# Kernel tuning notes

Hardware: AMD Instinct MI355X
Metric: run time of the kernel (lower is better)

Reference implementation:

```python
import jax, jax.numpy as jnp
import numpy as np

D = 64; H = 8; HD = 8; L = 3; FFN = 256
MAX_CHUNKS = 1024; MCL = 16


def rms_norm(x, w, eps=1e-6):
    return x * w * jax.lax.rsqrt(jnp.mean(x * x, axis=-1, keepdims=True) + eps)


def rope(x):
    # x: [B, S, H, HD]
    S, hd = x.shape[1], x.shape[-1]
    half = hd // 2
    freqs = 1.0 / (10000.0 ** (jnp.arange(half, dtype=x.dtype) * 2.0 / hd))
    ang = jnp.arange(S, dtype=x.dtype)[:, None] * freqs  # [S, half]
    cos = jnp.cos(ang)[None, :, None, :]
    sin = jnp.sin(ang)[None, :, None, :]
    x1, x2 = x[..., :half], x[..., half:]
    return jnp.concatenate([x1 * cos - x2 * sin, x1 * sin + x2 * cos], axis=-1)


def block(x, wq, wk, wv, wo, g1, g2, w1, w2):
    B, S, _ = x.shape
    h = rms_norm(x, g1)
    q = rope((h @ wq).reshape(B, S, H, HD))
    k = rope((h @ wk).reshape(B, S, H, HD))
    v = (h @ wv).reshape(B, S, H, HD)
    scores = jnp.einsum('bqhd,bkhd->bhqk', q, k) / jnp.sqrt(jnp.asarray(HD, x.dtype))
    causal = jnp.tril(jnp.ones((S, S), dtype=bool))
    scores = jnp.where(causal, scores, jnp.asarray(-1e30, x.dtype))
    attn = jax.nn.softmax(scores, axis=-1)
    o = jnp.einsum('bhqk,bkhd->bqhd', attn, v).reshape(B, S, D)
    x = x + o @ wo
    h2 = rms_norm(x, g2)
    return x + jax.nn.gelu(h2 @ w1, approximate=False) @ w2


def setup_inputs() -> dict:
    key = jax.random.key(0)
    ks = jax.random.split(key, 12)
    B, S = 4, 2048
    s = 1.0 / np.sqrt(D)
    return {
        'x': jax.random.normal(ks[0], (B, S, D), jnp.float32),
        'pad_token_vector': jax.random.normal(ks[1], (D,), jnp.float32),
        'x_ids': jax.random.randint(ks[2], (B, S), 0, 256),
        'pad_token_id': 257,
        'Wq': jax.random.normal(ks[3], (L, D, D), jnp.float32) * s,
        'Wk': jax.random.normal(ks[4], (L, D, D), jnp.float32) * s,
        'Wv': jax.random.normal(ks[5], (L, D, D), jnp.float32) * s,
        'Wo': jax.random.normal(ks[6], (L, D, D), jnp.float32) * s,
        'ln1': jnp.ones((L, D), jnp.float32),
        'ln2': jnp.ones((L, D), jnp.float32),
        'W1': jax.random.normal(ks[7], (L, D, FFN), jnp.float32) * s,
        'W2': jax.random.normal(ks[8], (L, FFN, D), jnp.float32) * (1.0 / np.sqrt(FFN)),
        'Whead': jax.random.normal(ks[9], (D, 2), jnp.float32) * s,
        'bhead': jnp.zeros((2,), jnp.float32),
    }


def reference(x, pad_token_vector, x_ids, pad_token_id, Wq, Wk, Wv, Wo, ln1, ln2, W1, W2, Whead, bhead):
    B, S, _ = x.shape
    h = x
    for l in range(L):
        h = block(h, Wq[l], Wk[l], Wv[l], Wo[l], ln1[l], ln2[l], W1[l], W2[l])
    logits = h @ Whead + bhead  # [B, S, 2]
    end_mask = logits[..., 0] > logits[..., 1]  # [B, S]
    t = jnp.arange(S)
    # fallback: if a row has no end, mark the last position as an end
    has_end = jnp.any(end_mask, axis=-1, keepdims=True)
    end_mask = jnp.where(has_end, end_mask, t[None, :] == S - 1)
    em = end_mask.astype(jnp.int32)
    num_ends = jnp.sum(em, axis=-1)                 # [B] = number of chunks
    chunk_id = jnp.cumsum(em, axis=-1) - em         # exclusive count of prior ends
    prev_end = jnp.concatenate([jnp.ones((B, 1), bool), end_mask[:, :-1]], axis=1)
    start_marker = jnp.where(prev_end, t[None, :], -1)
    start = jax.lax.associative_scan(jnp.maximum, start_marker, axis=-1)  # cummax -> chunk start per token
    pos = t[None, :] - start                        # position within chunk
    valid = (chunk_id < num_ends[:, None]) & (chunk_id < MAX_CHUNKS) & (pos < MCL)
    c_idx = jnp.where(valid, chunk_id, MAX_CHUNKS)  # invalid -> dummy chunk, sliced off
    p_idx = jnp.where(valid, pos, 0)
    b_idx = jnp.arange(B)[:, None]
    out = jnp.broadcast_to(pad_token_vector, (B, MAX_CHUNKS + 1, MCL, D))
    out = out.at[b_idx, c_idx, p_idx].set(h)[:, :MAX_CHUNKS]
    ids = jnp.full((B, MAX_CHUNKS + 1, MCL), pad_token_id, dtype=x_ids.dtype)
    ids = ids.at[b_idx, c_idx, p_idx].set(x_ids)[:, :MAX_CHUNKS]
    reg_term = jnp.mean(logits[..., 1])
    return out, ids, reg_term
```

## Files before the change

### kernel.cpp

```cpp
#include <hip/hip_runtime.h>
#include <math.h>

constexpr int D   = 64;
constexpr int H   = 8;
constexpr int HD  = 8;
constexpr int NL  = 3;
constexpr int FFNx= 256;
constexpr int Bb  = 4;
constexpr int Ss  = 2048;
constexpr int NT  = Bb * Ss;
constexpr int MAXC= 1024;
constexpr int MCL = 16;

constexpr int TPB  = 72;
constexpr int BPB  = 36;
constexpr int PBSZ = 2304;

constexpr size_t WX  = 0;
constexpr size_t WQ  = 524288;
constexpr size_t WKV = 2621440;
constexpr size_t WPB = 4194304;
constexpr size_t WL1 = 9764864;
constexpr size_t WEM = WL1 + NT;
constexpr size_t WINV= WEM + NT;
constexpr size_t WCT = WINV + Bb*MAXC*MCL;
constexpr size_t WST = WCT + Ss*4;

constexpr float LOG2E = 1.4426950408889634f;

typedef float v2f  __attribute__((ext_vector_type(2)));
typedef float f16v __attribute__((ext_vector_type(16)));
using ckv_t = const __attribute__((address_space(4))) f16v*;

__device__ __forceinline__ float rdlane(float v, int l) {
    return __builtin_bit_cast(float, __builtin_amdgcn_readlane(__builtin_bit_cast(int, v), l));
}

__global__ void k_init(const float* __restrict__ x, float* __restrict__ X,
                       float* __restrict__ ct, float* __restrict__ st) {
    int i = blockIdx.x * blockDim.x + threadIdx.x;
    constexpr int N4 = NT * D / 4;
    if (i < N4) ((float4*)X)[i] = ((const float4*)x)[i];
    if (i < Ss * 4) {
        int s = i >> 2, f = i & 3;
        const float fr[4] = {1.0f, 0.1f, 0.01f, 0.001f};
        float ang = (float)s * fr[f];
        ct[i] = cosf(ang);
        st[i] = sinf(ang);
    }
}

__global__ __launch_bounds__(256) void k_qkv(
    const float* __restrict__ X, const float* __restrict__ Wq,
    const float* __restrict__ Wk, const float* __restrict__ Wv,
    const float* __restrict__ g1, const float* __restrict__ ct,
    const float* __restrict__ st, float* __restrict__ Q,
    float* __restrict__ KV) {
    __shared__ float wq_s[D*D], wk_s[D*D], wv_s[D*D];
    __shared__ float g_s[D];
    int tid = threadIdx.x;
    for (int i = tid; i < D*D; i += 256) {
        wq_s[i] = Wq[i]; wk_s[i] = Wk[i]; wv_s[i] = Wv[i];
    }
    if (tid < D) g_s[tid] = g1[tid];
    __syncthreads();
    int w = tid >> 6, d = tid & 63;
    int t0 = blockIdx.x * 16;
    for (int it = 0; it < 4; ++it) {
        int t = t0 + it*4 + w;
        float xv = X[t*D + d];
        float ss = xv * xv;
        #pragma unroll
        for (int off = 32; off; off >>= 1) ss += __shfl_xor(ss, off);
        float r = 1.0f / sqrtf(ss * (1.0f/D) + 1e-6f);
        float h = xv * g_s[d] * r;
        float aq = 0.f, ak = 0.f, av = 0.f;
        #pragma unroll
        for (int j = 0; j < D; ++j) {
            float hj = rdlane(h, j);
            aq += hj * wq_s[j*D + d];
            ak += hj * wk_s[j*D + d];
            av += hj * wv_s[j*D + d];
        }
        int s  = t & (Ss - 1);
        int e  = d & 7;
        int fi = e & 3;
        float c  = ct[s*4 + fi];
        float sn = st[s*4 + fi];
        float pq = __shfl_xor(aq, 4);
        float pk = __shfl_xor(ak, 4);
        float rq, rk;
        if (e < 4) { rq = aq*c - pq*sn; rk = ak*c - pk*sn; }
        else       { rq = pq*sn + aq*c; rk = pk*sn + ak*c; }
        Q[t*D + d] = rq;
        int bq = t >> 11;
        int hh = d >> 3;
        float* kvp = KV + ((((size_t)(bq*H + hh))*Ss + s) << 4);
        kvp[e]     = rk;
        kvp[8 + e] = av;
    }
}

template<int DIAG>
__device__ __forceinline__ void attn_loop4(
    ckv_t kvs, int L, int rel0,
    const v2f* __restrict__ qp0, const v2f* __restrict__ qp1,
    v2f& l0, v2f& l1, v2f* __restrict__ o0, v2f* __restrict__ o1) {
    #pragma unroll 4
    for (int j = 0; j < 64; ++j) {
        f16v kv = kvs[j];
        v2f a1;
        a1  = qp1[0] * (v2f){kv[0], kv[0]};
        a1 += qp1[1] * (v2f){kv[1], kv[1]};
        a1 += qp1[2] * (v2f){kv[2], kv[2]};
        a1 += qp1[3] * (v2f){kv[3], kv[3]};
        a1 += qp1[4] * (v2f){kv[4], kv[4]};
        a1 += qp1[5] * (v2f){kv[5], kv[5]};
        a1 += qp1[6] * (v2f){kv[6], kv[6]};
        a1 += qp1[7] * (v2f){kv[7], kv[7]};
        if (DIAG == 2) {
            int rel = rel0 + j;
            if (rel > L)      a1.x = -1e30f;
            if (rel > L + 64) a1.y = -1e30f;
        }
        v2f p1;
        p1.x = __builtin_amdgcn_exp2f(a1.x);
        p1.y = __builtin_amdgcn_exp2f(a1.y);
        l1 += p1;
        o1[0] += p1 * (v2f){kv[8],  kv[8]};
        o1[1] += p1 * (v2f){kv[9],  kv[9]};
        o1[2] += p1 * (v2f){kv[10], kv[10]};
        o1[3] += p1 * (v2f){kv[11], kv[11]};
        o1[4] += p1 * (v2f){kv[12], kv[12]};
        o1[5] += p1 * (v2f){kv[13], kv[13]};
        o1[6] += p1 * (v2f){kv[14], kv[14]};
        o1[7] += p1 * (v2f){kv[15], kv[15]};
        if (DIAG != 2) {
            v2f a0;
            a0  = qp0[0] * (v2f){kv[0], kv[0]};
            a0 += qp0[1] * (v2f){kv[1], kv[1]};
            a0 += qp0[2] * (v2f){kv[2], kv[2]};
            a0 += qp0[3] * (v2f){kv[3], kv[3]};
            a0 += qp0[4] * (v2f){kv[4], kv[4]};
            a0 += qp0[5] * (v2f){kv[5], kv[5]};
            a0 += qp0[6] * (v2f){kv[6], kv[6]};
            a0 += qp0[7] * (v2f){kv[7], kv[7]};
            if (DIAG == 1) {
                int rel = rel0 + j;
                if (rel > L)      a0.x = -1e30f;
                if (rel > L + 64) a0.y = -1e30f;
            }
            v2f p0;
            p0.x = __builtin_amdgcn_exp2f(a0.x);
            p0.y = __builtin_amdgcn_exp2f(a0.y);
            l0 += p0;
            o0[0] += p0 * (v2f){kv[8],  kv[8]};
            o0[1] += p0 * (v2f){kv[9],  kv[9]};
            o0[2] += p0 * (v2f){kv[10], kv[10]};
            o0[3] += p0 * (v2f){kv[11], kv[11]};
            o0[4] += p0 * (v2f){kv[12], kv[12]};
            o0[5] += p0 * (v2f){kv[13], kv[13]};
            o0[6] += p0 * (v2f){kv[14], kv[14]};
            o0[7] += p0 * (v2f){kv[15], kv[15]};
        }
    }
}

__global__ __launch_bounds__(256) void k_attn2(
    const float* __restrict__ Qg, const float* __restrict__ KV,
    float* __restrict__ PB) {
    __shared__ float comb[2][PBSZ];
    int xcd  = blockIdx.x & 7;
    int slot = blockIdx.x >> 3;
    int bhg  = slot / BPB;
    int blk  = slot - bhg * BPB;
    int bh   = bhg * 8 + xcd;
    int wvu  = __builtin_amdgcn_readfirstlane(threadIdx.x >> 6);
    int pair = wvu >> 1;
    int half = wvu & 1;
    int widb = blk * 2 + pair;
    int L = threadIdx.x & 63;
    int rem = widb;
    int s = 0;
    while (rem >= 8 - (s >> 1)) { rem -= 8 - (s >> 1); ++s; }
    int t = (s >> 1) + rem;
    int b = bh >> 3, h = bh & 7;
    int qmin = t * 256;
    int k0 = s * 128 + half * 64;

    const float SC = 0.35355339059327373f * LOG2E;
    const float* qp = Qg + ((size_t)(b*Ss + qmin + L))*D + h*HD;
    float4 qa0 = *(const float4*)(qp);
    float4 qb0 = *(const float4*)(qp + 4);
    float4 qa1 = *(const float4*)(qp + 64*D);
    float4 qb1 = *(const float4*)(qp + 64*D + 4);
    float4 qa2 = *(const float4*)(qp + 128*D);
    float4 qb2 = *(const float4*)(qp + 128*D + 4);
    float4 qa3 = *(const float4*)(qp + 192*D);
    float4 qb3 = *(const float4*)(qp + 192*D + 4);
    v2f qp0[8], qp1[8];
    qp0[0] = (v2f){qa0.x*SC, qa1.x*SC};  qp1[0] = (v2f){qa2.x*SC, qa3.x*SC};
    qp0[1] = (v2f){qa0.y*SC, qa1.y*SC};  qp1[1] = (v2f){qa2.y*SC, qa3.y*SC};
    qp0[2] = (v2f){qa0.z*SC, qa1.z*SC};  qp1[2] = (v2f){qa2.z*SC, qa3.z*SC};
    qp0[3] = (v2f){qa0.w*SC, qa1.w*SC};  qp1[3] = (v2f){qa2.w*SC, qa3.w*SC};
    qp0[4] = (v2f){qb0.x*SC, qb1.x*SC};  qp1[4] = (v2f){qb2.x*SC, qb3.x*SC};
    qp0[5] = (v2f){qb0.y*SC, qb1.y*SC};  qp1[5] = (v2f){qb2.y*SC, qb3.y*SC};
    qp0[6] = (v2f){qb0.z*SC, qb1.z*SC};  qp1[6] = (v2f){qb2.z*SC, qb3.z*SC};
    qp0[7] = (v2f){qb0.w*SC, qb1.w*SC};  qp1[7] = (v2f){qb2.w*SC, qb3.w*SC};

    v2f l0 = (v2f){0.f, 0.f}, l1 = (v2f){0.f, 0.f};
    v2f o0[8], o1[8];
    #pragma unroll
    for (int e = 0; e < 8; ++e) { o0[e] = (v2f){0.f, 0.f}; o1[e] = (v2f){0.f, 0.f}; }

    ckv_t kvs = (ckv_t)(unsigned long long)(KV + (((size_t)bh*Ss + k0) << 4));
    if (s == 2*t)          attn_loop4<1>(kvs, L, half*64, qp0, qp1, l0, l1, o0, o1);
    else if (s == 2*t + 1) attn_loop4<2>(kvs, L, half*64, qp0, qp1, l0, l1, o0, o1);
    else                   attn_loop4<0>(kvs, L, half*64, qp0, qp1, l0, l1, o0, o1);

    if (half == 1) {
        comb[pair][L]       = l0.x;
        comb[pair][64 + L]  = l0.y;
        comb[pair][128 + L] = l1.x;
        comb[pair][192 + L] = l1.y;
        #pragma unroll
        for (int e = 0; e < 8; ++e) {
            comb[pair][256 + e*256 + L]       = o0[e].x;
            comb[pair][256 + e*256 + 64 + L]  = o0[e].y;
            comb[pair][256 + e*256 + 128 + L] = o1[e].x;
            comb[pair][256 + e*256 + 192 + L] = o1[e].y;
        }
    }
    __syncthreads();
    if (half == 0) {
        int pbidx = t*(t+1) + s;
        float* pb = PB + ((size_t)bh * TPB + pbidx) * PBSZ;
        pb[L]       = l0.x + comb[pair][L];
        pb[64 + L]  = l0.y + comb[pair][64 + L];
        pb[128 + L] = l1.x + comb[pair][128 + L];
        pb[192 + L] = l1.y + comb[pair][192 + L];
        #pragma unroll
        for (int e = 0; e < 8; ++e) {
            pb[256 + e*256 + L]       = o0[e].x + comb[pair][256 + e*256 + L];
            pb[256 + e*256 + 64 + L]  = o0[e].y + comb[pair][256 + e*256 + 64 + L];
            pb[256 + e*256 + 128 + L] = o1[e].x + comb[pair][256 + e*256 + 128 + L];
            pb[256 + e*256 + 192 + L] = o1[e].y + comb[pair][256 + e*256 + 192 + L];
        }
    }
}

template<bool HEAD>
__global__ __launch_bounds__(256) void k_cffn(
    const float* __restrict__ PB, float* __restrict__ X,
    const float* __restrict__ Wo, const float* __restrict__ g2,
    const float* __restrict__ W1, const float* __restrict__ W2,
    const float* __restrict__ Wh, const float* __restrict__ bhp,
    float* __restrict__ logit1, int* __restrict__ em) {
    __shared__ float wo_s[D*D];
    __shared__ float oT[16][65];
    __shared__ float xt[16][65];
    __shared__ __align__(16) float h2t[64][20];
    __shared__ float part[16][16];
    __shared__ float g_s[D];
    __shared__ __align__(16) float ult[FFNx][20];
    __shared__ float red[4][16][D];
    int tid = threadIdx.x;
    int gb  = blockIdx.x;
    int b    = gb >> 7;
    int tile = gb & 127;
    int t    = tile >> 4;
    int sq   = (tile & 15) << 4;
    int tok0 = b*Ss + t*256 + sq;
    for (int i = tid; i < D*D; i += 256) wo_s[i] = Wo[i];
    if (tid < D) g_s[tid] = g2[tid];

    {
        int h  = tid >> 5;
        int ql = (tid >> 1) & 15;
        int eh = tid & 1;
        int qs = sq + ql;
        int bh = b*8 + h;
        int nch = 2*(t+1);
        float Lx = 0.f;
        float O[4] = {0,0,0,0};
        for (int s3 = 0; s3 < nch; ++s3) {
            int idx = t*(t+1) + s3;
            const float* pb = PB + (size_t)(bh*TPB + idx) * PBSZ;
            Lx += pb[qs];
            #pragma unroll
            for (int e = 0; e < 4; ++e) O[e] += pb[256 + (eh*4 + e)*256 + qs];
        }
        float inv = 1.0f / Lx;
        #pragma unroll
        for (int e = 0; e < 4; ++e) oT[ql][h*8 + eh*4 + e] = O[e] * inv;
    }
    __syncthreads();
    {
        int d = tid & 63, wv = tid >> 6;
        #pragma unroll
        for (int k = 0; k < 4; ++k) {
            int tt = wv*4 + k;
            float a = 0.f;
            #pragma unroll
            for (int j = 0; j < D; ++j) a += oT[tt][j] * wo_s[j*D + d];
            xt[tt][d] = X[(size_t)(tok0 + tt)*D + d] + a;
        }
    }
    __syncthreads();
    int tk = tid >> 4, li = tid & 15;
    float x0 = xt[tk][li];
    float x1 = xt[tk][li + 16];
    float x2 = xt[tk][li + 32];
    float x3 = xt[tk][li + 48];
    part[tk][li] = x0*x0 + x1*x1 + x2*x2 + x3*x3;
    __syncthreads();
    if (tid < 16) {
        float s = 0.f;
        #pragma unroll
        for (int i = 0; i < 16; ++i) s += part[tid][i];
        part[tid][0] = 1.0f / sqrtf(s * (1.0f/D) + 1e-6f);
    }
    __syncthreads();
    float r = part[tk][0];
    h2t[li][tk]      = x0 * g_s[li]      * r;
    h2t[li + 16][tk] = x1 * g_s[li + 16] * r;
    h2t[li + 32][tk] = x2 * g_s[li + 32] * r;
    h2t[li + 48][tk] = x3 * g_s[li + 48] * r;
    __syncthreads();
    {
        int f = tid;
        v2f acc2[8];
        #pragma unroll
        for (int i = 0; i < 8; ++i) acc2[i] = (v2f){0.f, 0.f};
        for (int j = 0; j < D; ++j) {
            float wv = W1[j*FFNx + f];
            v2f wv2 = (v2f){wv, wv};
            const float4* hp = (const float4*)&h2t[j][0];
            float4 a0 = hp[0], a1 = hp[1], a2 = hp[2], a3 = hp[3];
            const v2f* a0v = (const v2f*)&a0;
            const v2f* a1v = (const v2f*)&a1;
            const v2f* a2v = (const v2f*)&a2;
            const v2f* a3v = (const v2f*)&a3;
            acc2[0] += a0v[0]*wv2;  acc2[1] += a0v[1]*wv2;
            acc2[2] += a1v[0]*wv2;  acc2[3] += a1v[1]*wv2;
            acc2[4] += a2v[0]*wv2;  acc2[5] += a2v[1]*wv2;
            acc2[6] += a3v[0]*wv2;  acc2[7] += a3v[1]*wv2;
        }
        #pragma unroll
        for (int i = 0; i < 8; ++i) {
            float ua = acc2[i].x;
            float ub = acc2[i].y;
            ua = 0.5f * ua * (1.0f + erff(ua * 0.70710678118654752f));
            ub = 0.5f * ub * (1.0f + erff(ub * 0.70710678118654752f));
            ult[f][2*i]     = ua;
            ult[f][2*i + 1] = ub;
        }
    }
    __syncthreads();
    {
        int d = tid & 63, fp = tid >> 6;
        v2f acc2[8];
        #pragma unroll
        for (int i = 0; i < 8; ++i) acc2[i] = (v2f){0.f, 0.f};
        for (int fo = 0; fo < 64; ++fo) {
            int f = fp*64 + fo;
            float wv = W2[f*D + d];
            v2f wv2 = (v2f){wv, wv};
            const float4* up = (const float4*)&ult[f][0];
            float4 u0 = up[0], u1 = up[1], u2 = up[2], u3 = up[3];
            const v2f* u0v = (const v2f*)&u0;
            const v2f* u1v = (const v2f*)&u1;
            const v2f* u2v = (const v2f*)&u2;
            const v2f* u3v = (const v2f*)&u3;
            acc2[0] += u0v[0]*wv2;  acc2[1] += u0v[1]*wv2;
            acc2[2] += u1v[0]*wv2;  acc2[3] += u1v[1]*wv2;
            acc2[4] += u2v[0]*wv2;  acc2[5] += u2v[1]*wv2;
            acc2[6] += u3v[0]*wv2;  acc2[7] += u3v[1]*wv2;
        }
        #pragma unroll
        for (int i = 0; i < 8; ++i) {
            red[fp][2*i][d]     = acc2[i].x;
            red[fp][2*i + 1][d] = acc2[i].y;
        }
        __syncthreads();
        int tk2 = tid >> 6;
        #pragma unroll
        for (int k = 0; k < 4; ++k) {
            int tt = tk2 + k*4;
            float sum = red[0][tt][d] + red[1][tt][d] + red[2][tt][d] + red[3][tt][d];
            float xf = xt[tt][d] + sum;
            X[(size_t)(tok0 + tt)*D + d] = xf;
            if (HEAD) {
                float p0 = xf * Wh[d*2];
                float p1 = xf * Wh[d*2 + 1];
                #pragma unroll
                for (int off = 32; off; off >>= 1) {
                    p0 += __shfl_xor(p0, off);
                    p1 += __shfl_xor(p1, off);
                }
                if (d == 0) {
                    float l0 = p0 + bhp[0], l1 = p1 + bhp[1];
                    em[tok0 + tt] = (l0 > l1) ? 1 : 0;
                    logit1[tok0 + tt] = l1;
                }
            }
        }
    }
}

__global__ __launch_bounds__(256) void k_scanreg(
    const int* __restrict__ em, int* __restrict__ inv,
    const float* __restrict__ logit1, float* __restrict__ outreg) {
    __shared__ int ssum[256], smax[256];
    __shared__ int sany, stot;
    int tid = threadIdx.x;
    if (blockIdx.x == Bb) {
        __shared__ float redf[256];
        float s = 0.f;
        for (int i = tid; i < NT; i += 256) s += logit1[i];
        redf[tid] = s;
        __syncthreads();
        for (int off = 128; off; off >>= 1) {
            if (tid < off) redf[tid] += redf[tid + off];
            __syncthreads();
        }
        if (tid == 0) *outreg = redf[0] * (1.0f / NT);
        return;
    }
    int b = blockIdx.x;
    int* invb = inv + b * (MAXC*MCL);
    for (int i = tid; i < MAXC*MCL; i += 256) invb[i] = -1;
    __syncthreads();
    const int* e = em + b*Ss;
    int base = tid * 8;
    int loc[8];
    int lsum = 0, lor = 0;
    #pragma unroll
    for (int i = 0; i < 8; ++i) { loc[i] = e[base + i]; lsum += loc[i]; lor |= loc[i]; }
    ssum[tid] = lor;
    __syncthreads();
    if (tid == 0) { int a = 0; for (int i = 0; i < 256; ++i) a |= ssum[i]; sany = a; }
    __syncthreads();
    int any = sany;
    __syncthreads();
    if (!any && tid == 255) { loc[7] = 1; lsum = 1; }
    int prev = (tid == 0) ? 1 : e[base - 1];
    if (!any && tid) prev = 0;
    int mk[8];
    int lmax = -1;
    #pragma unroll
    for (int i = 0; i < 8; ++i) {
        int pe = (i == 0) ? prev : loc[i - 1];
        if (i == 7 && !any && tid == 255) pe = e[base + 6];
        mk[i] = pe ? (base + i) : -1;
        lmax = max(lmax, mk[i]);
    }
    ssum[tid] = lsum; smax[tid] = lmax;
    __syncthreads();
    if (tid == 0) {
        int rs = 0, rm = -1;
        for (int i = 0; i < 256; ++i) {
            int ts = ssum[i], tm = smax[i];
            ssum[i] = rs; smax[i] = rm;
            rs += ts; rm = max(rm, tm);
        }
        stot = rs;
    }
    __syncthreads();
    int run = ssum[tid], rmax = smax[tid], tot = stot;
    #pragma unroll
    for (int i = 0; i < 8; ++i) {
        int s = base + i;
        rmax = max(rmax, mk[i]);
        int chunk = run;
        run += loc[i];
        int pos = s - rmax;
        bool valid = (chunk < tot) && (chunk < MAXC) && (pos < MCL);
        if (valid) invb[chunk * MCL + pos] = b*Ss + s;
    }
}

__global__ __launch_bounds__(256) void k_out(
    const float* __restrict__ X, const float* __restrict__ pad,
    const int* __restrict__ xids, const int* __restrict__ padid,
    const int* __restrict__ inv, float* __restrict__ out) {
    int i = blockIdx.x * blockDim.x + threadIdx.x;
    constexpr int NV4 = Bb * MAXC * MCL * D / 4;
    constexpr int NI4 = Bb * MAXC * MCL / 4;
    if (i < NV4) {
        int slot = i >> 4;
        int d4 = i & 15;
        int t = inv[slot];
        float4 v = (t >= 0) ? ((const float4*)X)[t*16 + d4]
                            : ((const float4*)pad)[d4];
        ((float4*)out)[i] = v;
    } else if (i < NV4 + NI4) {
        int j = i - NV4;
        float pv = (float)(*padid);
        int base = j * 4;
        int t0_ = inv[base], t1_ = inv[base+1], t2_ = inv[base+2], t3_ = inv[base+3];
        float4 v;
        v.x = (t0_ >= 0) ? (float)xids[t0_] : pv;
        v.y = (t1_ >= 0) ? (float)xids[t1_] : pv;
        v.z = (t2_ >= 0) ? (float)xids[t2_] : pv;
        v.w = (t3_ >= 0) ? (float)xids[t3_] : pv;
        ((float4*)out)[i] = v;
    }
}

extern "C" void kernel_launch(void* const* d_in, const int* in_sizes, int n_in,
                              void* d_out, int out_size, void* d_ws, size_t ws_size,
                              hipStream_t stream) {
    const float* x    = (const float*)d_in[0];
    const float* pad  = (const float*)d_in[1];
    const int*   xids = (const int*)  d_in[2];
    const int*   padid= (const int*)  d_in[3];
    const float* Wq   = (const float*)d_in[4];
    const float* Wk   = (const float*)d_in[5];
    const float* Wv   = (const float*)d_in[6];
    const float* Wo   = (const float*)d_in[7];
    const float* ln1  = (const float*)d_in[8];
    const float* ln2  = (const float*)d_in[9];
    const float* W1   = (const float*)d_in[10];
    const float* W2   = (const float*)d_in[11];
    const float* Wh   = (const float*)d_in[12];
    const float* bh   = (const float*)d_in[13];
    float* out = (float*)d_out;
    float* ws  = (float*)d_ws;

    float* X  = ws + WX;
    float* Qb = ws + WQ;
    float* KVb= ws + WKV;
    float* PBb= ws + WPB;
    float* L1b= ws + WL1;
    int*   EMb= (int*)(ws + WEM);
    int*   INVb=(int*)(ws + WINV);
    float* ct = ws + WCT;
    float* st = ws + WST;

    k_init<<<2048, 256, 0, stream>>>(x, X, ct, st);
    for (int l = 0; l < NL; ++l) {
        k_qkv <<<512, 256, 0, stream>>>(X, Wq + l*D*D, Wk + l*D*D, Wv + l*D*D,
                                        ln1 + l*D, ct, st, Qb, KVb);
        k_attn2<<<32*BPB, 256, 0, stream>>>(Qb, KVb, PBb);
        if (l == NL - 1)
            k_cffn<true ><<<512, 256, 0, stream>>>(PBb, X, Wo + l*D*D, ln2 + l*D,
                                                   W1 + l*D*FFNx, W2 + l*FFNx*D,
                                                   Wh, bh, L1b, EMb);
        else
            k_cffn<false><<<512, 256, 0, stream>>>(PBb, X, Wo + l*D*D, ln2 + l*D,
                                                   W1 + l*D*FFNx, W2 + l*FFNx*D,
                                                   nullptr, nullptr, nullptr, nullptr);
    }
    k_scanreg<<<Bb + 1, 256, 0, stream>>>(EMb, INVb, L1b,
                                          out + (size_t)Bb*MAXC*MCL*D + Bb*MAXC*MCL);
    k_out <<<(Bb*MAXC*MCL*D/4 + Bb*MAXC*MCL/4 + 255)/256, 256, 0, stream>>>(
        X, pad, xids, padid, INVb, out);
}
```

Measured before the change: 248.0 us.

## Fuse next layer's RMSNorm+QKV+RoPE projection into the FFN kernel epilogue

The FFN kernel for layers 0 and 1 now keeps its output tokens in registers and computes the next layer's RMSNorm, Q/K/V projections and RoPE directly, writing Q and KV buffers. This removes two separate k_qkv launches and the re-read of X from global memory. Shared memory is merged into one aliased buffer so the QKV weights fit. In exchange each FFN block reloads three 64x64 weight matrices and does extra serial work after the FFN.

```diff
diff --git a/kernel.cpp b/kernel.cpp
--- a/kernel.cpp
+++ b/kernel.cpp
@@ -249,21 +249,26 @@
     }
 }
 
-template<bool HEAD>
+template<bool HEAD, bool NEXTQ>
 __global__ __launch_bounds__(256) void k_cffn(
     const float* __restrict__ PB, float* __restrict__ X,
     const float* __restrict__ Wo, const float* __restrict__ g2,
     const float* __restrict__ W1, const float* __restrict__ W2,
     const float* __restrict__ Wh, const float* __restrict__ bhp,
-    float* __restrict__ logit1, int* __restrict__ em) {
-    __shared__ float wo_s[D*D];
-    __shared__ float oT[16][65];
-    __shared__ float xt[16][65];
-    __shared__ __align__(16) float h2t[64][20];
-    __shared__ float part[16][16];
-    __shared__ float g_s[D];
-    __shared__ __align__(16) float ult[FFNx][20];
-    __shared__ float red[4][16][D];
+    float* __restrict__ logit1, int* __restrict__ em,
+    const float* __restrict__ Wqn, const float* __restrict__ Wkn,
+    const float* __restrict__ Wvn, const float* __restrict__ g1n,
+    const float* __restrict__ ct, const float* __restrict__ st,
+    float* __restrict__ Q, float* __restrict__ KV) {
+    __shared__ __align__(16) float smem[16992];
+    float* wo_s = smem;
+    auto  oT   = (float(*)[65])(smem + 4096);
+    auto  xt   = (float(*)[65])(smem + 5136);
+    auto  h2t  = (float(*)[20])(smem + 6176);
+    auto  part = (float(*)[16])(smem + 7456);
+    float* g_s = smem + 7712;
+    auto  ult  = (float(*)[20])(smem + 7776);
+    auto  red  = (float(*)[16][64])(smem + 12896);
     int tid = threadIdx.x;
     int gb  = blockIdx.x;
     int b    = gb >> 7;
@@ -357,14 +362,15 @@
         }
     }
     __syncthreads();
+    float xfr[4];
+    int d2 = tid & 63, fp = tid >> 6;
     {
-        int d = tid & 63, fp = tid >> 6;
         v2f acc2[8];
         #pragma unroll
         for (int i = 0; i < 8; ++i) acc2[i] = (v2f){0.f, 0.f};
         for (int fo = 0; fo < 64; ++fo) {
             int f = fp*64 + fo;
-            float wv = W2[f*D + d];
+            float wv = W2[f*D + d2];
             v2f wv2 = (v2f){wv, wv};
             const float4* up = (const float4*)&ult[f][0];
             float4 u0 = up[0], u1 = up[1], u2 = up[2], u3 = up[3];
@@ -379,31 +385,79 @@
         }
         #pragma unroll
         for (int i = 0; i < 8; ++i) {
-            red[fp][2*i][d]     = acc2[i].x;
-            red[fp][2*i + 1][d] = acc2[i].y;
+            red[fp][2*i][d2]     = acc2[i].x;
+            red[fp][2*i + 1][d2] = acc2[i].y;
         }
         __syncthreads();
         int tk2 = tid >> 6;
         #pragma unroll
         for (int k = 0; k < 4; ++k) {
             int tt = tk2 + k*4;
-            float sum = red[0][tt][d] + red[1][tt][d] + red[2][tt][d] + red[3][tt][d];
-            float xf = xt[tt][d] + sum;
-            X[(size_t)(tok0 + tt)*D + d] = xf;
+            float sum = red[0][tt][d2] + red[1][tt][d2] + red[2][tt][d2] + red[3][tt][d2];
+            float xf = xt[tt][d2] + sum;
+            xfr[k] = xf;
+            X[(size_t)(tok0 + tt)*D + d2] = xf;
             if (HEAD) {
-                float p0 = xf * Wh[d*2];
-                float p1 = xf * Wh[d*2 + 1];
+                float p0 = xf * Wh[d2*2];
+                float p1 = xf * Wh[d2*2 + 1];
                 #pragma unroll
                 for (int off = 32; off; off >>= 1) {
                     p0 += __shfl_xor(p0, off);
                     p1 += __shfl_xor(p1, off);
                 }
-                if (d == 0) {
+                if (d2 == 0) {
                     float l0 = p0 + bhp[0], l1 = p1 + bhp[1];
                     em[tok0 + tt] = (l0 > l1) ? 1 : 0;
                     logit1[tok0 + tt] = l1;
                 }
             }
+        }
+    }
+    if (NEXTQ) {
+        __syncthreads();
+        float* wq_s = smem;
+        float* wk_s = smem + 4096;
+        float* wv_s = smem + 8192;
+        float* g1_s = smem + 12288;
+        for (int i = tid; i < D*D; i += 256) {
+            wq_s[i] = Wqn[i]; wk_s[i] = Wkn[i]; wv_s[i] = Wvn[i];
+        }
+        if (tid < D) g1_s[tid] = g1n[tid];
+        __syncthreads();
+        int wvi = tid >> 6, d = tid & 63;
+        #pragma unroll
+        for (int k = 0; k < 4; ++k) {
+            int tglob = tok0 + wvi + k*4;
+            float xv = xfr[k];
+            float ss = xv * xv;
+            #pragma unroll
+            for (int off = 32; off; off >>= 1) ss += __shfl_xor(ss, off);
+            float rq_ = 1.0f / sqrtf(ss * (1.0f/D) + 1e-6f);
+            float h = xv * g1_s[d] * rq_;
+            float aq = 0.f, ak = 0.f, av = 0.f;
+            #pragma unroll
+            for (int j = 0; j < D; ++j) {
+                float hj = rdlane(h, j);
+                aq += hj * wq_s[j*D + d];
+                ak += hj * wk_s[j*D + d];
+                av += hj * wv_s[j*D + d];
+            }
+            int s  = tglob & (Ss - 1);
+            int e  = d & 7;
+            int fi = e & 3;
+            float c  = ct[s*4 + fi];
+            float sn = st[s*4 + fi];
+            float pq = __shfl_xor(aq, 4);
+            float pk = __shfl_xor(ak, 4);
+            float rq, rk;
+            if (e < 4) { rq = aq*c - pq*sn; rk = ak*c - pk*sn; }
+            else       { rq = pq*sn + aq*c; rk = pk*sn + ak*c; }
+            Q[(size_t)tglob*D + d] = rq;
+            int bq = tglob >> 11;
+            int hh = d >> 3;
+            float* kvp = KV + ((((size_t)(bq*H + hh))*Ss + s) << 4);
+            kvp[e]     = rk;
+            kvp[8 + e] = av;
         }
     }
 }
@@ -539,18 +593,20 @@
     float* st = ws + WST;
 
     k_init<<<2048, 256, 0, stream>>>(x, X, ct, st);
+    k_qkv <<<512, 256, 0, stream>>>(X, Wq, Wk, Wv, ln1, ct, st, Qb, KVb);
     for (int l = 0; l < NL; ++l) {
-        k_qkv <<<512, 256, 0, stream>>>(X, Wq + l*D*D, Wk + l*D*D, Wv + l*D*D,
-                                        ln1 + l*D, ct, st, Qb, KVb);
         k_attn2<<<32*BPB, 256, 0, stream>>>(Qb, KVb, PBb);
         if (l == NL - 1)
-            k_cffn<true ><<<512, 256, 0, stream>>>(PBb, X, Wo + l*D*D, ln2 + l*D,
-                                                   W1 + l*D*FFNx, W2 + l*FFNx*D,
-                                                   Wh, bh, L1b, EMb);
+            k_cffn<true , false><<<512, 256, 0, stream>>>(
+                PBb, X, Wo + l*D*D, ln2 + l*D, W1 + l*D*FFNx, W2 + l*FFNx*D,
+                Wh, bh, L1b, EMb,
+                nullptr, nullptr, nullptr, nullptr, ct, st, Qb, KVb);
         else
-            k_cffn<false><<<512, 256, 0, stream>>>(PBb, X, Wo + l*D*D, ln2 + l*D,
-                                                   W1 + l*D*FFNx, W2 + l*FFNx*D,
-                                                   nullptr, nullptr, nullptr, nullptr);
+            k_cffn<false, true ><<<512, 256, 0, stream>>>(
+                PBb, X, Wo + l*D*D, ln2 + l*D, W1 + l*D*FFNx, W2 + l*FFNx*D,
+                nullptr, nullptr, nullptr, nullptr,
+                Wq + (l+1)*D*D, Wk + (l+1)*D*D, Wv + (l+1)*D*D, ln1 + (l+1)*D,
+                ct, st, Qb, KVb);
     }
     k_scanreg<<<Bb + 1, 256, 0, stream>>>(EMb, INVb, L1b,
                                           out + (size_t)Bb*MAXC*MCL*D + Bb*MAXC*MCL);
```

After: 318.9 us. 28.6% more time.
